# Optimization experiments

Hardware: AMD Instinct MI355X
Metric: run time of the kernel (lower is better)

Reference implementation:

```python
import jax, jax.numpy as jnp
import numpy as np

B, L, D_MODEL = 4, 2048, 512
N_HEAD, D_K, D_V = 8, 64, 64
LN_EPS = 1e-5


def setup_inputs() -> dict:
    key = jax.random.key(0)
    ks = jax.random.split(key, 12)
    std_qk = np.sqrt(2.0 / (D_MODEL + D_K)).astype(np.float32)
    std_v = np.sqrt(2.0 / (D_MODEL + D_V)).astype(np.float32)
    return {
        "q": jax.random.normal(ks[0], (B, L, D_MODEL), jnp.float32),
        "k": jax.random.normal(ks[1], (B, L, D_MODEL), jnp.float32),
        "v": jax.random.normal(ks[2], (B, L, D_MODEL), jnp.float32),
        "mask": jax.random.randint(ks[3], (B, L, L), 0, 2) == 1,
        "wq_w": jax.random.normal(ks[4], (N_HEAD * D_K, D_MODEL), jnp.float32) * std_qk,
        "wq_b": jnp.zeros((N_HEAD * D_K,), jnp.float32),
        "wk_w": jax.random.normal(ks[5], (N_HEAD * D_K, D_MODEL), jnp.float32) * std_qk,
        "wk_b": jnp.zeros((N_HEAD * D_K,), jnp.float32),
        "wv_w": jax.random.normal(ks[6], (N_HEAD * D_V, D_MODEL), jnp.float32) * std_v,
        "wv_b": jnp.zeros((N_HEAD * D_V,), jnp.float32),
        "fc_w": jax.random.normal(ks[7], (D_MODEL, N_HEAD * D_V), jnp.float32) * np.sqrt(2.0 / (D_MODEL + N_HEAD * D_V)).astype(np.float32),
        "fc_b": jnp.zeros((D_MODEL,), jnp.float32),
        "ln_g": jnp.ones((D_MODEL,), jnp.float32),
        "ln_b": jnp.zeros((D_MODEL,), jnp.float32),
    }


def _layer_norm(x, g, b):
    mu = jnp.mean(x, axis=-1, keepdims=True)
    var = jnp.var(x, axis=-1, keepdims=True)
    return (x - mu) * jax.lax.rsqrt(var + LN_EPS) * g + b


def reference(q, k, v, mask, wq_w, wq_b, wk_w, wk_b, wv_w, wv_b, fc_w, fc_b, ln_g, ln_b):
    b, lq, _ = q.shape
    residual = q
    qh = (q @ wq_w.T + wq_b).reshape(b, lq, N_HEAD, D_K)
    kh = (k @ wk_w.T + wk_b).reshape(b, lq, N_HEAD, D_K)
    vh = (v @ wv_w.T + wv_b).reshape(b, lq, N_HEAD, D_V)
    # scores: [b, h, lq, lk]
    attn = jnp.einsum("bqhd,bkhd->bhqk", qh, kh) / jnp.asarray(D_K ** 0.5, qh.dtype)
    attn = jnp.where(mask[:, None, :, :], -jnp.inf, attn)
    attn = jax.nn.softmax(attn, axis=-1)
    out = jnp.einsum("bhqk,bkhd->bqhd", attn, vh).reshape(b, lq, N_HEAD * D_V)
    out = out @ fc_w.T + fc_b  # dropout is identity in eval
    out = _layer_norm(out + residual, ln_g, ln_b)
    # match torch attn layout: (n_head*b, lq, lk), head-major
    attn_flat = jnp.transpose(attn, (1, 0, 2, 3)).reshape(N_HEAD * b, lq, lq)
    return (out, attn_flat)
```

## Files before the change

kernel.cpp:

```cpp
#include <hip/hip_runtime.h>
#include <hip/hip_bf16.h>
#include <cstdint>

#define B_ 4
#define L_ 2048
#define DM 512
#define H_ 8
#define T_ (B_*L_)
#define LDP 72

typedef _Float16 f16;
typedef _Float16 f16x8 __attribute__((ext_vector_type(8)));
typedef _Float16 f16x4v __attribute__((ext_vector_type(4)));
typedef float f32x4 __attribute__((ext_vector_type(4)));

__global__ void k_detect(const unsigned char* __restrict__ mask, int* __restrict__ flag) {
    __shared__ int s_any;
    if (threadIdx.x == 0) s_any = 0;
    __syncthreads();
    int any = 0;
    for (int i = threadIdx.x; i < 4096; i += 256)
        if ((i & 3) && mask[i]) any = 1;
    if (any) atomicOr(&s_any, 1);
    __syncthreads();
    if (threadIdx.x == 0) *flag = s_any;
}

__global__ void k_packmask(const void* __restrict__ mask, const int* __restrict__ flag,
                           unsigned long long* __restrict__ mw) {
    int gid = blockIdx.x * 256 + threadIdx.x;
    int wid = gid >> 6;
    int lane = gid & 63;
    long long idx = (long long)wid * 64 + lane;
    int v;
    if (*flag) v = ((const unsigned char*)mask)[idx];
    else       v = ((const int*)mask)[idx];
    unsigned long long m = __ballot(v != 0);
    if (lane == 0) mw[wid] = m;
}

__global__ void k_cvt(const float* __restrict__ in, f16* __restrict__ out, int n) {
    int i = (blockIdx.x * 256 + threadIdx.x) * 4;
    if (i >= n) return;
    float4 v = *(const float4*)&in[i];
    f16x4v o = { (f16)v.x, (f16)v.y, (f16)v.z, (f16)v.w };
    *(f16x4v*)&out[i] = o;
}

template<int LAYOUT>
__launch_bounds__(256, 2)
__global__ void k_gemm(const f16* __restrict__ A, const f16* __restrict__ W,
                       const float* __restrict__ bias,
                       float* __restrict__ outf, f16* __restrict__ outh) {
    const int K = DM, N = DM;
    __shared__ f16 As[64][LDP];
    __shared__ f16 Ws[64][LDP];
    int m0 = blockIdx.x * 64;
    int n0 = blockIdx.y * 64;
    int t = threadIdx.x;
    int w = t >> 6, l = t & 63;
    int lr = l & 15, lkof = (l >> 4) * 8, lg = (l >> 4) * 4;
    f32x4 acc[4] = {};
    int row[2], c8[2];
    f16x8 ar[2], wr[2];
#pragma unroll
    for (int i = 0; i < 2; ++i) {
        int chunk = t + i * 256;
        row[i] = chunk >> 3; c8[i] = (chunk & 7) * 8;
        ar[i] = *(const f16x8*)&A[(long long)(m0 + row[i]) * K + c8[i]];
        wr[i] = *(const f16x8*)&W[(long long)(n0 + row[i]) * K + c8[i]];
    }
    for (int k0 = 0; k0 < K; k0 += 64) {
        __syncthreads();
#pragma unroll
        for (int i = 0; i < 2; ++i) {
            *(f16x8*)&As[row[i]][c8[i]] = ar[i];
            *(f16x8*)&Ws[row[i]][c8[i]] = wr[i];
        }
        __syncthreads();
        if (k0 + 64 < K) {
#pragma unroll
            for (int i = 0; i < 2; ++i) {
                ar[i] = *(const f16x8*)&A[(long long)(m0 + row[i]) * K + k0 + 64 + c8[i]];
                wr[i] = *(const f16x8*)&W[(long long)(n0 + row[i]) * K + k0 + 64 + c8[i]];
            }
        }
#pragma unroll
        for (int ks = 0; ks < 2; ++ks) {
            f16x8 a = *(const f16x8*)&As[w * 16 + lr][ks * 32 + lkof];
#pragma unroll
            for (int nt = 0; nt < 4; ++nt) {
                f16x8 b = *(const f16x8*)&Ws[nt * 16 + lr][ks * 32 + lkof];
                acc[nt] = __builtin_amdgcn_mfma_f32_16x16x32_f16(a, b, acc[nt], 0, 0, 0);
            }
        }
    }
#pragma unroll
    for (int nt = 0; nt < 4; ++nt) {
        int j = n0 + nt * 16 + lr;
        float bj = bias[j];
#pragma unroll
        for (int r = 0; r < 4; ++r) {
            int m = m0 + w * 16 + lg + r;
            float v = acc[nt][r] + bj;
            if (LAYOUT == 0) {
                outf[(long long)m * N + j] = v;
            } else {
                int bb = m >> 11, pos = m & (L_ - 1);
                int hh = j >> 6, d = j & 63;
                outh[((long long)(bb * H_ + hh) * L_ + pos) * 64 + d] = (f16)v;
            }
        }
    }
}

__launch_bounds__(256, 2)
__global__ void k_attn(const f16* __restrict__ QH, const f16* __restrict__ KH,
                       const f16* __restrict__ VH, const unsigned long long* __restrict__ mw,
                       float* __restrict__ attn_out, f16* __restrict__ Obuf) {
    __shared__ f16 Qs[64][LDP];
    __shared__ f16 Ks[64][LDP];
    __shared__ f16 Vt[64][LDP];
    __shared__ f16 Ps[4][16][LDP];
    int bid = blockIdx.x;
    int rb = bid & 31;
    int bh = bid >> 5;
    int b = bh >> 3, h = bh & 7;
    int t = threadIdx.x, w = t >> 6, l = t & 63;
    int lr = l & 15, lkof = (l >> 4) * 8, lg = (l >> 4) * 4;
    const f16* Qp = QH + (long long)bh * L_ * 64 + (long long)rb * 64 * 64;
    const f16* Kp = KH + (long long)bh * L_ * 64;
    const f16* Vp = VH + (long long)bh * L_ * 64;
    int row[2], c8[2];
#pragma unroll
    for (int i = 0; i < 2; ++i) {
        int chunk = t + i * 256;
        row[i] = chunk >> 3; c8[i] = (chunk & 7) * 8;
        *(f16x8*)&Qs[row[i]][c8[i]] = *(const f16x8*)&Qp[row[i] * 64 + c8[i]];
    }
    __syncthreads();
    f16x8 qf[2];
    qf[0] = *(const f16x8*)&Qs[w * 16 + lr][lkof];
    qf[1] = *(const f16x8*)&Qs[w * 16 + lr][32 + lkof];

    float lrun[4] = {0.f, 0.f, 0.f, 0.f};
    const unsigned long long* mwrow = mw + ((long long)b * L_ + rb * 64) * (L_ / 64);

    f16x8 kr[2];
#pragma unroll
    for (int i = 0; i < 2; ++i)
        kr[i] = *(const f16x8*)&Kp[row[i] * 64 + c8[i]];
    for (int c = 0; c < 32; ++c) {
        __syncthreads();
#pragma unroll
        for (int i = 0; i < 2; ++i)
            *(f16x8*)&Ks[row[i]][c8[i]] = kr[i];
        __syncthreads();
        if (c < 31) {
#pragma unroll
            for (int i = 0; i < 2; ++i)
                kr[i] = *(const f16x8*)&Kp[((c + 1) * 64 + row[i]) * 64 + c8[i]];
        }
        f32x4 s[4] = {};
#pragma unroll
        for (int ks = 0; ks < 2; ++ks) {
#pragma unroll
            for (int nt = 0; nt < 4; ++nt) {
                f16x8 bfr = *(const f16x8*)&Ks[nt * 16 + lr][ks * 32 + lkof];
                s[nt] = __builtin_amdgcn_mfma_f32_16x16x32_f16(qf[ks], bfr, s[nt], 0, 0, 0);
            }
        }
#pragma unroll
        for (int j = 0; j < 4; ++j) {
            int lq = w * 16 + lg + j;
            unsigned long long wmask = mwrow[lq * 32 + c];
            float sum = 0.f;
#pragma unroll
            for (int nt = 0; nt < 4; ++nt) {
                int bit = nt * 16 + lr;
                float e = ((wmask >> bit) & 1ull) ? 0.f : __expf(s[nt][j] * 0.125f - 4.f);
                sum += e;
            }
#pragma unroll
            for (int off = 1; off < 16; off <<= 1)
                sum += __shfl_xor(sum, off);
            lrun[j] += sum;
        }
    }
    float inv[4];
#pragma unroll
    for (int j = 0; j < 4; ++j) inv[j] = 1.f / lrun[j];

    f32x4 oacc[4] = {};
    float* aout = attn_out + ((long long)(h * B_ + b) * L_ + (long long)rb * 64) * L_;

    f16x8 vr[2];
#pragma unroll
    for (int i = 0; i < 2; ++i) {
        kr[i] = *(const f16x8*)&Kp[row[i] * 64 + c8[i]];
        vr[i] = *(const f16x8*)&Vp[row[i] * 64 + c8[i]];
    }
    for (int c = 0; c < 32; ++c) {
        __syncthreads();
#pragma unroll
        for (int i = 0; i < 2; ++i) {
            *(f16x8*)&Ks[row[i]][c8[i]] = kr[i];
            int kx = (c8[i] >> 3) << 3;
#pragma unroll
            for (int ee = 0; ee < 8; ++ee)
                Vt[c8[i] + ee][row[i] ^ (kx & 56)] = vr[i][ee];
        }
        __syncthreads();
        if (c < 31) {
#pragma unroll
            for (int i = 0; i < 2; ++i) {
                kr[i] = *(const f16x8*)&Kp[((c + 1) * 64 + row[i]) * 64 + c8[i]];
                vr[i] = *(const f16x8*)&Vp[((c + 1) * 64 + row[i]) * 64 + c8[i]];
            }
        }
        f32x4 s[4] = {};
#pragma unroll
        for (int ks = 0; ks < 2; ++ks) {
#pragma unroll
            for (int nt = 0; nt < 4; ++nt) {
                f16x8 bfr = *(const f16x8*)&Ks[nt * 16 + lr][ks * 32 + lkof];
                s[nt] = __builtin_amdgcn_mfma_f32_16x16x32_f16(qf[ks], bfr, s[nt], 0, 0, 0);
            }
        }
#pragma unroll
        for (int j = 0; j < 4; ++j) {
            int lq = w * 16 + lg + j;
            unsigned long long wmask = mwrow[lq * 32 + c];
#pragma unroll
            for (int nt = 0; nt < 4; ++nt) {
                int bit = nt * 16 + lr;
                float e = ((wmask >> bit) & 1ull) ? 0.f : __expf(s[nt][j] * 0.125f - 4.f);
                float p = e * inv[j];
                aout[(long long)lq * L_ + c * 64 + nt * 16 + lr] = p;
                Ps[w][lg + j][nt * 16 + lr] = (f16)p;
            }
        }
        __syncthreads();
#pragma unroll
        for (int ks = 0; ks < 2; ++ks) {
            f16x8 ap = *(const f16x8*)&Ps[w][lr][ks * 32 + lkof];
#pragma unroll
            for (int nt = 0; nt < 4; ++nt) {
                int r = nt * 16 + lr;
                int kxr = ((r >> 3) & 7) << 3;
                f16x8 bv = *(const f16x8*)&Vt[r][(ks * 32 + lkof) ^ kxr];
                oacc[nt] = __builtin_amdgcn_mfma_f32_16x16x32_f16(ap, bv, oacc[nt], 0, 0, 0);
            }
        }
    }
#pragma unroll
    for (int nt = 0; nt < 4; ++nt) {
#pragma unroll
        for (int r = 0; r < 4; ++r) {
            int lq = rb * 64 + w * 16 + lg + r;
            Obuf[((long long)b * L_ + lq) * DM + h * 64 + nt * 16 + lr] = (f16)oacc[nt][r];
        }
    }
}

__global__ void k_ln(const float* __restrict__ fc, const float* __restrict__ res,
                     const float* __restrict__ g, const float* __restrict__ bb,
                     float* __restrict__ out) {
    int row = blockIdx.x * 4 + (threadIdx.x >> 6);
    int l = threadIdx.x & 63;
    const float* x = fc + (size_t)row * DM + l * 8;
    const float* r = res + (size_t)row * DM + l * 8;
    float4 a0 = *(const float4*)x;
    float4 a1 = *(const float4*)(x + 4);
    float4 r0 = *(const float4*)r;
    float4 r1 = *(const float4*)(r + 4);
    float v[8] = {a0.x + r0.x, a0.y + r0.y, a0.z + r0.z, a0.w + r0.w,
                  a1.x + r1.x, a1.y + r1.y, a1.z + r1.z, a1.w + r1.w};
    float s = 0.f, s2 = 0.f;
#pragma unroll
    for (int i = 0; i < 8; ++i) { s += v[i]; s2 += v[i] * v[i]; }
#pragma unroll
    for (int off = 1; off < 64; off <<= 1) {
        s += __shfl_xor(s, off);
        s2 += __shfl_xor(s2, off);
    }
    float mean = s * (1.f / 512.f);
    float var = s2 * (1.f / 512.f) - mean * mean;
    float rstd = rsqrtf(var + 1e-5f);
    const float* gp = g + l * 8;
    const float* bp = bb + l * 8;
    float4 g0 = *(const float4*)gp, g1 = *(const float4*)(gp + 4);
    float4 b0 = *(const float4*)bp, b1 = *(const float4*)(bp + 4);
    float og[8] = {g0.x, g0.y, g0.z, g0.w, g1.x, g1.y, g1.z, g1.w};
    float ob[8] = {b0.x, b0.y, b0.z, b0.w, b1.x, b1.y, b1.z, b1.w};
    float o[8];
#pragma unroll
    for (int i = 0; i < 8; ++i) o[i] = (v[i] - mean) * rstd * og[i] + ob[i];
    float4 w0 = {o[0], o[1], o[2], o[3]};
    float4 w1 = {o[4], o[5], o[6], o[7]};
    float* op = out + (size_t)row * DM + l * 8;
    *(float4*)op = w0;
    *(float4*)(op + 4) = w1;
}

extern "C" void kernel_launch(void* const* d_in, const int* in_sizes, int n_in,
                              void* d_out, int out_size, void* d_ws, size_t ws_size,
                              hipStream_t stream) {
    const float* q    = (const float*)d_in[0];
    const float* k    = (const float*)d_in[1];
    const float* v    = (const float*)d_in[2];
    const void*  mask = d_in[3];
    const float* wq_w = (const float*)d_in[4];
    const float* wq_b = (const float*)d_in[5];
    const float* wk_w = (const float*)d_in[6];
    const float* wk_b = (const float*)d_in[7];
    const float* wv_w = (const float*)d_in[8];
    const float* wv_b = (const float*)d_in[9];
    const float* fc_w = (const float*)d_in[10];
    const float* fc_b = (const float*)d_in[11];
    const float* ln_g = (const float*)d_in[12];
    const float* ln_b = (const float*)d_in[13];

    float* out      = (float*)d_out;
    float* attn_out = out + (size_t)T_ * DM;

    char* ws = (char*)d_ws;
    constexpr size_t SZ_MASKW  = (size_t)B_ * L_ * (L_ / 64) * 8;
    constexpr size_t SZ_F16_TD = (size_t)T_ * DM * 2;
    constexpr size_t SZ_F16_W  = (size_t)DM * DM * 2;
    size_t off = 0;
    auto take = [&](size_t bytes) { char* p = ws + off; off = (off + bytes + 255) & ~(size_t)255; return p; };
    unsigned long long* maskw = (unsigned long long*)take(SZ_MASKW);
    int*  flag  = (int*)take(256);
    f16*  qf    = (f16*)take(SZ_F16_TD);
    f16*  kf    = (f16*)take(SZ_F16_TD);
    f16*  vf    = (f16*)take(SZ_F16_TD);
    f16*  wqf   = (f16*)take(SZ_F16_W);
    f16*  wkf   = (f16*)take(SZ_F16_W);
    f16*  wvf   = (f16*)take(SZ_F16_W);
    f16*  fcf   = (f16*)take(SZ_F16_W);
    f16*  QHp   = (f16*)take(SZ_F16_TD);
    f16*  KHp   = (f16*)take(SZ_F16_TD);
    f16*  VHp   = (f16*)take(SZ_F16_TD);
    f16*  Obuf  = (f16*)take(SZ_F16_TD);
    float* FCout = (float*)take((size_t)T_ * DM * 4);
    (void)ws_size; (void)in_sizes; (void)n_in; (void)out_size;

    k_detect<<<1, 256, 0, stream>>>((const unsigned char*)mask, flag);
    k_packmask<<<(B_ * L_ * L_ / 64) / 4, 256, 0, stream>>>(mask, flag, maskw);

    k_cvt<<<(T_ * DM / 4) / 256, 256, 0, stream>>>(q, qf, T_ * DM);
    k_cvt<<<(T_ * DM / 4) / 256, 256, 0, stream>>>(k, kf, T_ * DM);
    k_cvt<<<(T_ * DM / 4) / 256, 256, 0, stream>>>(v, vf, T_ * DM);
    k_cvt<<<(DM * DM / 4) / 256, 256, 0, stream>>>(wq_w, wqf, DM * DM);
    k_cvt<<<(DM * DM / 4) / 256, 256, 0, stream>>>(wk_w, wkf, DM * DM);
    k_cvt<<<(DM * DM / 4) / 256, 256, 0, stream>>>(wv_w, wvf, DM * DM);
    k_cvt<<<(DM * DM / 4) / 256, 256, 0, stream>>>(fc_w, fcf, DM * DM);

    dim3 gg(T_ / 64, DM / 64);
    k_gemm<1><<<gg, 256, 0, stream>>>(qf, wqf, wq_b, nullptr, QHp);
    k_gemm<1><<<gg, 256, 0, stream>>>(kf, wkf, wk_b, nullptr, KHp);
    k_gemm<1><<<gg, 256, 0, stream>>>(vf, wvf, wv_b, nullptr, VHp);

    k_attn<<<B_ * H_ * (L_ / 64), 256, 0, stream>>>(QHp, KHp, VHp, maskw, attn_out, Obuf);

    k_gemm<0><<<gg, 256, 0, stream>>>(Obuf, fcf, fc_b, FCout, nullptr);

    k_ln<<<T_ / 4, 256, 0, stream>>>(FCout, q, ln_g, ln_b, out);
}
```

Measured before the change: 881.5 us.

## Rewrite projection GEMM with async LDS loads, double buffering, swizzle; batch conversions

Replaces the projection and output GEMM with a 128x64 tile that uses global_load_lds direct-to-LDS copies into double-buffered, XOR-swizzled shared memory, so loads overlap the MFMA work. The seven fp32-to-fp16 conversion launches become two batched launches. The attention kernel swaps a block-wide barrier before the P·V step for a per-wave LDS wait plus sched_barrier, since each wave reads only its own Ps slice. The gains are fewer launches and better GEMM overlap, at the cost of more LDS per block and reliance on the async-load ordering being correct.

```diff
diff --git a/kernel.cpp b/kernel.cpp
--- a/kernel.cpp
+++ b/kernel.cpp
@@ -13,6 +13,10 @@
 typedef _Float16 f16x8 __attribute__((ext_vector_type(8)));
 typedef _Float16 f16x4v __attribute__((ext_vector_type(4)));
 typedef float f32x4 __attribute__((ext_vector_type(4)));
+
+#define GLOAD16(gp, lp) __builtin_amdgcn_global_load_lds( \
+    (const __attribute__((address_space(1))) void*)(gp),  \
+    (__attribute__((address_space(3))) void*)(lp), 16, 0, 0)
 
 __global__ void k_detect(const unsigned char* __restrict__ mask, int* __restrict__ flag) {
     __shared__ int s_any;
@@ -39,76 +43,99 @@
     if (lane == 0) mw[wid] = m;
 }
 
-__global__ void k_cvt(const float* __restrict__ in, f16* __restrict__ out, int n) {
+__global__ void k_cvt3(const float* __restrict__ a, const float* __restrict__ b,
+                       const float* __restrict__ c,
+                       f16* __restrict__ oa, f16* __restrict__ ob, f16* __restrict__ oc) {
     int i = (blockIdx.x * 256 + threadIdx.x) * 4;
-    if (i >= n) return;
-    float4 v = *(const float4*)&in[i];
+    const float* src = blockIdx.y == 0 ? a : blockIdx.y == 1 ? b : c;
+    f16* dst = blockIdx.y == 0 ? oa : blockIdx.y == 1 ? ob : oc;
+    float4 v = *(const float4*)&src[i];
     f16x4v o = { (f16)v.x, (f16)v.y, (f16)v.z, (f16)v.w };
-    *(f16x4v*)&out[i] = o;
+    *(f16x4v*)&dst[i] = o;
+}
+__global__ void k_cvt4(const float* __restrict__ a, const float* __restrict__ b,
+                       const float* __restrict__ c, const float* __restrict__ d,
+                       f16* __restrict__ oa, f16* __restrict__ ob,
+                       f16* __restrict__ oc, f16* __restrict__ od) {
+    int i = (blockIdx.x * 256 + threadIdx.x) * 4;
+    const float* src = blockIdx.y == 0 ? a : blockIdx.y == 1 ? b : blockIdx.y == 2 ? c : d;
+    f16* dst = blockIdx.y == 0 ? oa : blockIdx.y == 1 ? ob : blockIdx.y == 2 ? oc : od;
+    float4 v = *(const float4*)&src[i];
+    f16x4v o = { (f16)v.x, (f16)v.y, (f16)v.z, (f16)v.w };
+    *(f16x4v*)&dst[i] = o;
 }
 
 template<int LAYOUT>
 __launch_bounds__(256, 2)
-__global__ void k_gemm(const f16* __restrict__ A, const f16* __restrict__ W,
-                       const float* __restrict__ bias,
-                       float* __restrict__ outf, f16* __restrict__ outh) {
-    const int K = DM, N = DM;
-    __shared__ f16 As[64][LDP];
-    __shared__ f16 Ws[64][LDP];
-    int m0 = blockIdx.x * 64;
-    int n0 = blockIdx.y * 64;
-    int t = threadIdx.x;
-    int w = t >> 6, l = t & 63;
-    int lr = l & 15, lkof = (l >> 4) * 8, lg = (l >> 4) * 4;
-    f32x4 acc[4] = {};
-    int row[2], c8[2];
-    f16x8 ar[2], wr[2];
-#pragma unroll
-    for (int i = 0; i < 2; ++i) {
-        int chunk = t + i * 256;
-        row[i] = chunk >> 3; c8[i] = (chunk & 7) * 8;
-        ar[i] = *(const f16x8*)&A[(long long)(m0 + row[i]) * K + c8[i]];
-        wr[i] = *(const f16x8*)&W[(long long)(n0 + row[i]) * K + c8[i]];
-    }
-    for (int k0 = 0; k0 < K; k0 += 64) {
-        __syncthreads();
-#pragma unroll
-        for (int i = 0; i < 2; ++i) {
-            *(f16x8*)&As[row[i]][c8[i]] = ar[i];
-            *(f16x8*)&Ws[row[i]][c8[i]] = wr[i];
-        }
-        __syncthreads();
-        if (k0 + 64 < K) {
-#pragma unroll
-            for (int i = 0; i < 2; ++i) {
-                ar[i] = *(const f16x8*)&A[(long long)(m0 + row[i]) * K + k0 + 64 + c8[i]];
-                wr[i] = *(const f16x8*)&W[(long long)(n0 + row[i]) * K + k0 + 64 + c8[i]];
-            }
-        }
+__global__ void k_gemm2(const f16* __restrict__ A, const f16* __restrict__ W,
+                        const float* __restrict__ bias,
+                        float* __restrict__ outf, f16* __restrict__ outh) {
+    constexpr int K = DM;
+    __shared__ f16 As[2][128 * 64];
+    __shared__ f16 Ws[2][64 * 64];
+    const int m0 = blockIdx.x * 128;
+    const int n0 = blockIdx.y * 64;
+    const int t = threadIdx.x;
+    const int wv = t >> 6, l = t & 63;
+    const int lr = l & 15, g = l >> 4, lg = g * 4;
+    const int sr = l >> 3;
+    const int sc = 8 * ((l & 7) ^ sr);
+    f32x4 acc[2][4] = {};
+
+    auto stage = [&](int buf, int kt) {
+        const long long k0 = kt * 64;
+#pragma unroll
+        for (int j = 0; j < 4; ++j) {
+            int r = wv * 32 + j * 8;
+            GLOAD16(A + (long long)(m0 + r + sr) * K + k0 + sc, &As[buf][r * 64]);
+        }
+#pragma unroll
+        for (int j = 0; j < 2; ++j) {
+            int r = wv * 16 + j * 8;
+            GLOAD16(W + (long long)(n0 + r + sr) * K + k0 + sc, &Ws[buf][r * 64]);
+        }
+    };
+
+    stage(0, 0);
+    __syncthreads();
+    for (int kt = 0; kt < 8; ++kt) {
+        const int cur = kt & 1;
+        if (kt < 7) stage(cur ^ 1, kt + 1);
 #pragma unroll
         for (int ks = 0; ks < 2; ++ks) {
-            f16x8 a = *(const f16x8*)&As[w * 16 + lr][ks * 32 + lkof];
-#pragma unroll
-            for (int nt = 0; nt < 4; ++nt) {
-                f16x8 b = *(const f16x8*)&Ws[nt * 16 + lr][ks * 32 + lkof];
-                acc[nt] = __builtin_amdgcn_mfma_f32_16x16x32_f16(a, b, acc[nt], 0, 0, 0);
-            }
-        }
+            f16x8 af[2];
+#pragma unroll
+            for (int mt = 0; mt < 2; ++mt) {
+                int row = wv * 32 + mt * 16 + lr;
+                af[mt] = *(const f16x8*)&As[cur][row * 64 + ((ks * 32 + g * 8) ^ ((row & 7) << 3))];
+            }
+#pragma unroll
+            for (int nt = 0; nt < 4; ++nt) {
+                int row = nt * 16 + lr;
+                f16x8 bf = *(const f16x8*)&Ws[cur][row * 64 + ((ks * 32 + g * 8) ^ ((row & 7) << 3))];
+#pragma unroll
+                for (int mt = 0; mt < 2; ++mt)
+                    acc[mt][nt] = __builtin_amdgcn_mfma_f32_16x16x32_f16(af[mt], bf, acc[mt][nt], 0, 0, 0);
+            }
+        }
+        __syncthreads();
     }
 #pragma unroll
     for (int nt = 0; nt < 4; ++nt) {
         int j = n0 + nt * 16 + lr;
         float bj = bias[j];
 #pragma unroll
-        for (int r = 0; r < 4; ++r) {
-            int m = m0 + w * 16 + lg + r;
-            float v = acc[nt][r] + bj;
-            if (LAYOUT == 0) {
-                outf[(long long)m * N + j] = v;
-            } else {
-                int bb = m >> 11, pos = m & (L_ - 1);
-                int hh = j >> 6, d = j & 63;
-                outh[((long long)(bb * H_ + hh) * L_ + pos) * 64 + d] = (f16)v;
+        for (int mt = 0; mt < 2; ++mt) {
+#pragma unroll
+            for (int r = 0; r < 4; ++r) {
+                int m = m0 + wv * 32 + mt * 16 + lg + r;
+                float vv = acc[mt][nt][r] + bj;
+                if (LAYOUT == 0) {
+                    outf[(long long)m * DM + j] = vv;
+                } else {
+                    int bb = m >> 11, pos = m & (L_ - 1);
+                    outh[((long long)(bb * H_ + (j >> 6)) * L_ + pos) * 64 + (j & 63)] = (f16)vv;
+                }
             }
         }
     }
@@ -240,7 +267,8 @@
                 Ps[w][lg + j][nt * 16 + lr] = (f16)p;
             }
         }
-        __syncthreads();
+        asm volatile("s_waitcnt lgkmcnt(0)" ::: "memory");
+        __builtin_amdgcn_sched_barrier(0);
 #pragma unroll
         for (int ks = 0; ks < 2; ++ks) {
             f16x8 ap = *(const f16x8*)&Ps[w][lr][ks * 32 + lkof];
@@ -349,22 +377,19 @@
     k_detect<<<1, 256, 0, stream>>>((const unsigned char*)mask, flag);
     k_packmask<<<(B_ * L_ * L_ / 64) / 4, 256, 0, stream>>>(mask, flag, maskw);
 
-    k_cvt<<<(T_ * DM / 4) / 256, 256, 0, stream>>>(q, qf, T_ * DM);
-    k_cvt<<<(T_ * DM / 4) / 256, 256, 0, stream>>>(k, kf, T_ * DM);
-    k_cvt<<<(T_ * DM / 4) / 256, 256, 0, stream>>>(v, vf, T_ * DM);
-    k_cvt<<<(DM * DM / 4) / 256, 256, 0, stream>>>(wq_w, wqf, DM * DM);
-    k_cvt<<<(DM * DM / 4) / 256, 256, 0, stream>>>(wk_w, wkf, DM * DM);
-    k_cvt<<<(DM * DM / 4) / 256, 256, 0, stream>>>(wv_w, wvf, DM * DM);
-    k_cvt<<<(DM * DM / 4) / 256, 256, 0, stream>>>(fc_w, fcf, DM * DM);
-
-    dim3 gg(T_ / 64, DM / 64);
-    k_gemm<1><<<gg, 256, 0, stream>>>(qf, wqf, wq_b, nullptr, QHp);
-    k_gemm<1><<<gg, 256, 0, stream>>>(kf, wkf, wk_b, nullptr, KHp);
-    k_gemm<1><<<gg, 256, 0, stream>>>(vf, wvf, wv_b, nullptr, VHp);
+    dim3 g3((T_ * DM / 4) / 256, 3);
+    k_cvt3<<<g3, 256, 0, stream>>>(q, k, v, qf, kf, vf);
+    dim3 g4((DM * DM / 4) / 256, 4);
+    k_cvt4<<<g4, 256, 0, stream>>>(wq_w, wk_w, wv_w, fc_w, wqf, wkf, wvf, fcf);
+
+    dim3 gg(T_ / 128, DM / 64);
+    k_gemm2<1><<<gg, 256, 0, stream>>>(qf, wqf, wq_b, nullptr, QHp);
+    k_gemm2<1><<<gg, 256, 0, stream>>>(kf, wkf, wk_b, nullptr, KHp);
+    k_gemm2<1><<<gg, 256, 0, stream>>>(vf, wvf, wv_b, nullptr, VHp);
 
     k_attn<<<B_ * H_ * (L_ / 64), 256, 0, stream>>>(QHp, KHp, VHp, maskw, attn_out, Obuf);
 
-    k_gemm<0><<<gg, 256, 0, stream>>>(Obuf, fcf, fc_b, FCout, nullptr);
+    k_gemm2<0><<<gg, 256, 0, stream>>>(Obuf, fcf, fc_b, FCout, nullptr);
 
     k_ln<<<T_ / 4, 256, 0, stream>>>(FCout, q, ln_g, ln_b, out);
 }
```

After: 850.7 us. -3.5%, faster.
